# Optimization experiments

Measured on AMD Instinct MI355X. Metric: run time of the kernel, lower is better.

## Reference

```python
import jax, jax.numpy as jnp
import numpy as np

WIN = (7, 7)
HW = WIN[0] * WIN[1]          # 49
C = 128
NUM_HEAD = 4
HEAD_DIM = C // NUM_HEAD
SCALE = HEAD_DIM ** -0.5
BS = 16384
NUM_WIN = 1024


def _relative_position_index():
    coords = np.stack(np.meshgrid(np.arange(WIN[0]), np.arange(WIN[1]), indexing='ij'))
    coords = coords.reshape(2, -1)                      # (2, hw)
    rel = coords[:, :, None] - coords[:, None, :]       # (2, hw, hw)
    rel = rel.transpose(1, 2, 0).copy()                 # (hw, hw, 2)
    rel[:, :, 0] += WIN[0] - 1
    rel[:, :, 1] += WIN[1] - 1
    rel[:, :, 0] *= 2 * WIN[1] - 1
    return rel.sum(-1).astype(np.int32)                 # (hw, hw)


def setup_inputs() -> dict:
    key = jax.random.key(0)
    ks = jax.random.split(key, 7)
    x = jax.random.normal(ks[0], (BS, HW, C), dtype=jnp.float32)
    mask = jax.random.normal(ks[1], (NUM_WIN, HW, HW), dtype=jnp.float32)
    qkv_w = jax.random.normal(ks[2], (3 * C, C), dtype=jnp.float32) * (C ** -0.5)
    qkv_b = jnp.zeros((3 * C,), dtype=jnp.float32)
    proj_w = jax.random.normal(ks[3], (C, C), dtype=jnp.float32) * (C ** -0.5)
    proj_b = jnp.zeros((C,), dtype=jnp.float32)
    num_rel = (2 * WIN[0] - 1) * (2 * WIN[1] - 1)       # 169
    bias_table = jax.random.normal(ks[4], (num_rel, NUM_HEAD), dtype=jnp.float32) * 0.02
    rel_index = jnp.asarray(_relative_position_index())
    return {"x": x, "mask": mask, "qkv_w": qkv_w, "qkv_b": qkv_b,
            "proj_w": proj_w, "proj_b": proj_b, "bias_table": bias_table,
            "rel_index": rel_index}


def reference(x, mask, qkv_w, qkv_b, proj_w, proj_b, bias_table, rel_index):
    bs, hw, c = x.shape
    qkv = x @ qkv_w.T + qkv_b                                   # (bs, hw, 3C)
    qkv = qkv.reshape(bs, hw, 3, NUM_HEAD, HEAD_DIM)
    qkv = jnp.transpose(qkv, (2, 0, 3, 1, 4))                   # (3, bs, H, hw, hd)
    q, k, v = qkv[0] * SCALE, qkv[1], qkv[2]
    attn = jnp.einsum('bhqd,bhkd->bhqk', q, k)                  # (bs, H, hw, hw)
    # gathered relative position bias: (hw, hw, H) -> (H, hw, hw)
    rel_bias = bias_table[rel_index.reshape(-1)].reshape(hw, hw, NUM_HEAD)
    attn = attn + jnp.transpose(rel_bias, (2, 0, 1))[None]
    nW = mask.shape[0]
    attn = attn.reshape(bs // nW, nW, NUM_HEAD, hw, hw) + mask[None, :, None]
    attn = attn.reshape(bs, NUM_HEAD, hw, hw)
    attn = jax.nn.softmax(attn, axis=-1)
    out = jnp.einsum('bhqk,bhkd->bhqd', attn, v)                # (bs, H, hw, hd)
    out = jnp.transpose(out, (0, 2, 1, 3)).reshape(bs, hw, c)
    return out @ proj_w.T + proj_b
```

## Files before the change

kernel.cpp:

```cpp
#include <hip/hip_runtime.h>
#include <hip/hip_bf16.h>

#define THREADS 512
#define WPB 8
#define NWIN 16384
#define NBLK (NWIN / WPB)

typedef short bf16x8 __attribute__((ext_vector_type(8)));
typedef float f32x4 __attribute__((ext_vector_type(4)));

#define XAP 136
#define QKP 264
#define VTP 72

#define XA0_OFF 0
#define XA1_OFF 6664
#define QK_OFF  13328
#define VT_OFF  26264
#define POOL_USHORTS 35480

#define LOG2E 1.4426950408889634f
#define SCALE_Q 0.17677669529663689f

#define COMB_FLOATS (1024 * 4 * 49 * 52)
#define COMB_BYTES  ((size_t)COMB_FLOATS * 4)
#define WQ_USHORTS (96 * 64 * 8)
#define WP_USHORTS (32 * 64 * 8)

static __device__ __forceinline__ unsigned short f2bf(float x) {
    union { __hip_bfloat16 b; unsigned short u; } c;
    c.b = __float2bfloat16(x);
    return c.u;
}
static __device__ __forceinline__ unsigned pack2bf(float lo, float hi) {
    return (unsigned)f2bf(lo) | ((unsigned)f2bf(hi) << 16);
}
static __device__ __forceinline__ ushort4 cvt4(float4 v) {
    ushort4 u; u.x = f2bf(v.x); u.y = f2bf(v.y); u.z = f2bf(v.z); u.w = f2bf(v.w);
    return u;
}

__global__ __launch_bounds__(512)
void prep_weights(const float* __restrict__ qkv_w, const float* __restrict__ proj_w,
                  unsigned short* __restrict__ wq, unsigned short* __restrict__ wp)
{
    const int t = blockIdx.x * 512 + threadIdx.x;
    if (t < 96 * 64) {
        const int lane = t & 63, g = t >> 6;
        const int l16 = lane & 15, lg = lane >> 4;
        const int ks = g & 3, wn = g >> 2;
        const int ch = wn * 16 + l16;
        const float s = (ch < 128) ? (SCALE_Q * LOG2E) : 1.0f;
        const float* p = qkv_w + (size_t)ch * 128 + ks * 32 + lg * 8;
        bf16x8 f;
#pragma unroll
        for (int j = 0; j < 8; ++j) f[j] = (short)f2bf(p[j] * s);
        *(bf16x8*)&wq[(size_t)t * 8] = f;
    } else if (t < 96 * 64 + 32 * 64) {
        const int t2 = t - 96 * 64;
        const int lane = t2 & 63, g = t2 >> 6;
        const int l16 = lane & 15, lg = lane >> 4;
        const int ks = g & 3, wv = g >> 2;
        const float* p = proj_w + (size_t)(wv * 16 + l16) * 128 + ks * 32 + lg * 8;
        bf16x8 f;
#pragma unroll
        for (int j = 0; j < 8; ++j) f[j] = (short)f2bf(p[j]);
        *(bf16x8*)&wp[(size_t)t2 * 8] = f;
    }
}

__global__ __launch_bounds__(512)
void prep_comb(const float* __restrict__ mask, const float* __restrict__ bias_table,
               const int* __restrict__ rel_index, float* __restrict__ comb)
{
    const unsigned t = blockIdx.x * 512 + threadIdx.x;
    if (t >= 1024u * 4u * 49u * 49u) return;
    const unsigned wi = t / 9604u;
    const unsigned r1 = t - wi * 9604u;
    const unsigned h  = r1 / 2401u;
    const unsigned r2 = r1 - h * 2401u;
    const unsigned qt = r2 / 49u;
    const unsigned kt = r2 - qt * 49u;
    const float m = mask[wi * 2401u + r2];
    const float b = bias_table[rel_index[r2] * 4 + h];
    comb[(((size_t)wi * 4u + h) * 49u + qt) * 52u + kt] = (m + b) * LOG2E;
}

__global__ __launch_bounds__(THREADS, 4)
void winattn_kernel(const float* __restrict__ x, const float* __restrict__ comb,
                    const unsigned short* __restrict__ wq, const unsigned short* __restrict__ wpr,
                    const float* __restrict__ qkv_b, const float* __restrict__ proj_b,
                    float* __restrict__ out)
{
    __shared__ __align__(16) unsigned short pool[POOL_USHORTS];

    const int tid  = threadIdx.x;
    const int wave = tid >> 6;
    const int lane = tid & 63;
    const int lg   = lane >> 4;
    const int l16  = lane & 15;
    const int h    = wave >> 1;
    const int mh   = wave & 1;

    const float4 pb = *(const float4*)(proj_b + wave * 16 + lg * 4);

    const int idxA = l16 + 2 * (lane & 16);
    const int idxB = idxA + 16;
    const bool hiSel = (lane & 32) != 0;

    const int win0 = blockIdx.x * WPB;

    {
        unsigned* p32 = (unsigned*)pool;
        for (int i = QK_OFF / 2 + tid; i < (QK_OFF + 12936 + 9216) / 2; i += THREADS)
            p32[i] = 0;
    }
#pragma unroll
    for (int it = 0; it < 4; ++it) {
        const int e = it * 2048 + tid * 4;
        if (e < 6272) {
            float4 v = *(const float4*)(x + (size_t)win0 * 6272 + e);
            *(ushort4*)&pool[XA0_OFF + (e >> 7) * XAP + (e & 127)] = cvt4(v);
        }
    }
    __syncthreads();

    for (int w = 0; w < WPB; ++w) {
        const int win = win0 + w;
        const bool pf = (w + 1 < WPB);
        const int xaC = (w & 1) ? XA1_OFF : XA0_OFF;
        const int xaN = (w & 1) ? XA0_OFF : XA1_OFF;

        if (pf) {
            const float* xp1 = x + (size_t)(win + 1) * 6272;
#pragma unroll
            for (int it = 0; it < 4; ++it) {
                const int e = it * 2048 + tid * 4;
                if (e < 6272) {
                    float4 v = *(const float4*)(xp1 + e);
                    *(ushort4*)&pool[xaN + (e >> 7) * XAP + (e & 127)] = cvt4(v);
                }
            }
        }

        {
            uintptr_t wqu = (uintptr_t)wq;
            asm volatile("" : "+s"(wqu));
            const unsigned short* wqx = (const unsigned short*)wqu;
#pragma unroll
            for (int nt = 0; nt < 3; ++nt) {
                bf16x8 wB[4];
#pragma unroll
                for (int ks = 0; ks < 4; ++ks)
                    wB[ks] = *(const bf16x8*)&wqx[(size_t)(((wave * 3 + nt) * 4 + ks) * 64 + lane) * 8];
                const int chB = wave * 48 + nt * 16;
                float4 qb4;
                if (chB < 256) {
                    qb4 = *(const float4*)(qkv_b + chB + lg * 4);
                    if (chB < 128) { qb4.x *= SCALE_Q * LOG2E; qb4.y *= SCALE_Q * LOG2E;
                                     qb4.z *= SCALE_Q * LOG2E; qb4.w *= SCALE_Q * LOG2E; }
                } else {
                    qb4.x = qkv_b[chB + l16];
                }
#pragma unroll
                for (int mt = 0; mt < 4; ++mt) {
                    bf16x8 xf[4];
#pragma unroll
                    for (int ks = 0; ks < 4; ++ks)
                        xf[ks] = *(const bf16x8*)&pool[xaC + (mt * 16 + l16) * XAP + ks * 32 + lg * 8];
                    f32x4 acc = (f32x4){0.f, 0.f, 0.f, 0.f};
                    if (chB < 256) {
#pragma unroll
                        for (int ks = 0; ks < 4; ++ks)
                            acc = __builtin_amdgcn_mfma_f32_16x16x32_bf16(wB[ks], xf[ks], acc, 0, 0, 0);
                        const int tok = mt * 16 + l16;
                        if (tok < 49) {
                            float4 v; v.x = acc[0] + qb4.x; v.y = acc[1] + qb4.y;
                            v.z = acc[2] + qb4.z; v.w = acc[3] + qb4.w;
                            *(ushort4*)&pool[QK_OFF + tok * QKP + chB + lg * 4] = cvt4(v);
                        }
                    } else {
#pragma unroll
                        for (int ks = 0; ks < 4; ++ks)
                            acc = __builtin_amdgcn_mfma_f32_16x16x32_bf16(xf[ks], wB[ks], acc, 0, 0, 0);
                        const float vb = qb4.x;
                        float4 v; v.x = acc[0] + vb; v.y = acc[1] + vb;
                        v.z = acc[2] + vb; v.w = acc[3] + vb;
                        *(ushort4*)&pool[VT_OFF + (chB - 256 + l16) * VTP + mt * 16 + lg * 4] = cvt4(v);
                    }
                }
            }
        }
        __syncthreads();

        const float* combW = comb + ((size_t)((win & 1023) * 4 + h)) * (49 * 52);
        float inv[2];
        unsigned pk[2][4][2];
#pragma unroll
        for (int nt = 0; nt < 2; ++nt) {
            const int qt = mh * 32 + nt * 16 + l16;
            const int qrow = (qt > 48) ? 48 : qt;
            const float* crow = combW + qrow * 52;
            const float4 c0 = *(const float4*)(crow + lg * 4);
            const float4 c1 = *(const float4*)(crow + 16 + lg * 4);
            const float4 c2 = *(const float4*)(crow + 32 + lg * 4);
            const float  c3 = crow[48];
            const bf16x8 bq = *(const bf16x8*)&pool[QK_OFF + qt * QKP + h * 32 + lg * 8];
            f32x4 S[4];
            __builtin_amdgcn_s_setprio(1);
#pragma unroll
            for (int mt = 0; mt < 4; ++mt) {
                const bf16x8 ak = *(const bf16x8*)&pool[QK_OFF + (mt * 16 + l16) * QKP + 128 + h * 32 + lg * 8];
                S[mt] = __builtin_amdgcn_mfma_f32_16x16x32_bf16(ak, bq, (f32x4){0.f,0.f,0.f,0.f}, 0, 0, 0);
            }
            __builtin_amdgcn_s_setprio(0);
            float lv[12];
            lv[0] = S[0][0] + c0.x; lv[1] = S[0][1] + c0.y;
            lv[2] = S[0][2] + c0.z; lv[3] = S[0][3] + c0.w;
            lv[4] = S[1][0] + c1.x; lv[5] = S[1][1] + c1.y;
            lv[6] = S[1][2] + c1.z; lv[7] = S[1][3] + c1.w;
            lv[8] = S[2][0] + c2.x; lv[9] = S[2][1] + c2.y;
            lv[10] = S[2][2] + c2.z; lv[11] = S[2][3] + c2.w;
            const float lv3 = (lg == 0) ? (S[3][0] + c3) : -1e30f;

            float sum = 0.f;
#pragma unroll
            for (int i = 0; i < 12; ++i) {
                const float p = exp2f(lv[i]);
                lv[i] = p;
                sum += p;
            }
            const float p3 = exp2f(lv3);
            sum += p3;
            sum += __shfl_xor(sum, 16);
            sum += __shfl_xor(sum, 32);
            inv[nt] = 1.0f / sum;
            pk[nt][0][0] = pack2bf(lv[0], lv[1]);  pk[nt][0][1] = pack2bf(lv[2], lv[3]);
            pk[nt][1][0] = pack2bf(lv[4], lv[5]);  pk[nt][1][1] = pack2bf(lv[6], lv[7]);
            pk[nt][2][0] = pack2bf(lv[8], lv[9]);  pk[nt][2][1] = pack2bf(lv[10], lv[11]);
            pk[nt][3][0] = pack2bf(p3, 0.f);       pk[nt][3][1] = 0u;
        }

        f32x4 O[2][2];
#pragma unroll
        for (int i = 0; i < 2; ++i)
#pragma unroll
            for (int j = 0; j < 2; ++j) O[i][j] = (f32x4){0.f, 0.f, 0.f, 0.f};
#pragma unroll
        for (int kh = 0; kh < 2; ++kh) {
            bf16x8 bv[2];
#pragma unroll
            for (int i = 0; i < 2; ++i)
                bv[i] = *(const bf16x8*)&pool[VT_OFF + (h * 32 + i * 16 + l16) * VTP + kh * 32 + lg * 8];
#pragma unroll
            for (int j = 0; j < 2; ++j) {
                const unsigned s0a = (unsigned)__shfl((int)pk[j][2 * kh + 0][0], idxA, 64);
                const unsigned s0b = (unsigned)__shfl((int)pk[j][2 * kh + 1][0], idxA, 64);
                const unsigned s1a = (unsigned)__shfl((int)pk[j][2 * kh + 0][1], idxA, 64);
                const unsigned s1b = (unsigned)__shfl((int)pk[j][2 * kh + 1][1], idxA, 64);
                const unsigned s2a = (unsigned)__shfl((int)pk[j][2 * kh + 0][0], idxB, 64);
                const unsigned s2b = (unsigned)__shfl((int)pk[j][2 * kh + 1][0], idxB, 64);
                const unsigned s3a = (unsigned)__shfl((int)pk[j][2 * kh + 0][1], idxB, 64);
                const unsigned s3b = (unsigned)__shfl((int)pk[j][2 * kh + 1][1], idxB, 64);
                unsigned pau[4];
                pau[0] = hiSel ? s0b : s0a;
                pau[1] = hiSel ? s1b : s1a;
                pau[2] = hiSel ? s2b : s2a;
                pau[3] = hiSel ? s3b : s3a;
                const bf16x8 pa = *(const bf16x8*)pau;
                __builtin_amdgcn_s_setprio(1);
#pragma unroll
                for (int i = 0; i < 2; ++i)
                    O[i][j] = __builtin_amdgcn_mfma_f32_16x16x32_bf16(bv[i], pa, O[i][j], 0, 0, 0);
                __builtin_amdgcn_s_setprio(0);
            }
        }
#pragma unroll
        for (int j = 0; j < 2; ++j) {
            const int tok = mh * 32 + j * 16 + l16;
            if (tok < 49) {
#pragma unroll
                for (int i = 0; i < 2; ++i) {
                    float4 v;
                    v.x = O[i][j][0] * inv[j]; v.y = O[i][j][1] * inv[j];
                    v.z = O[i][j][2] * inv[j]; v.w = O[i][j][3] * inv[j];
                    *(ushort4*)&pool[xaC + tok * XAP + h * 32 + i * 16 + lg * 4] = cvt4(v);
                }
            }
        }
        __syncthreads();

        bf16x8 wp_[4];
        {
            uintptr_t wpu = (uintptr_t)wpr;
            asm volatile("" : "+s"(wpu));
            const unsigned short* wpx = (const unsigned short*)wpu;
#pragma unroll
            for (int ks = 0; ks < 4; ++ks)
                wp_[ks] = *(const bf16x8*)&wpx[(size_t)((wave * 4 + ks) * 64 + lane) * 8];
        }
#pragma unroll
        for (int nt4 = 0; nt4 < 4; ++nt4) {
            f32x4 pc = (f32x4){0.f, 0.f, 0.f, 0.f};
#pragma unroll
            for (int ks = 0; ks < 4; ++ks) {
                const bf16x8 bfr = *(const bf16x8*)&pool[xaC + (nt4 * 16 + l16) * XAP + ks * 32 + lg * 8];
                pc = __builtin_amdgcn_mfma_f32_16x16x32_bf16(wp_[ks], bfr, pc, 0, 0, 0);
            }
            const int tok = nt4 * 16 + l16;
            if (tok < 49) {
                float4 o;
                o.x = pc[0] + pb.x; o.y = pc[1] + pb.y;
                o.z = pc[2] + pb.z; o.w = pc[3] + pb.w;
                *(float4*)(out + ((size_t)win * 49 + tok) * 128 + wave * 16 + lg * 4) = o;
            }
        }
        __syncthreads();
    }
}

extern "C" void kernel_launch(void* const* d_in, const int* in_sizes, int n_in,
                              void* d_out, int out_size, void* d_ws, size_t ws_size,
                              hipStream_t stream) {
    const float* x          = (const float*)d_in[0];
    const float* mask       = (const float*)d_in[1];
    const float* qkv_w      = (const float*)d_in[2];
    const float* qkv_b      = (const float*)d_in[3];
    const float* proj_w     = (const float*)d_in[4];
    const float* proj_b     = (const float*)d_in[5];
    const float* bias_table = (const float*)d_in[6];
    const int*   rel_index  = (const int*)d_in[7];
    float* out = (float*)d_out;
    (void)in_sizes; (void)n_in; (void)ws_size; (void)out_size;

    float* comb = (float*)d_ws;
    unsigned short* wq = (unsigned short*)((char*)d_ws + COMB_BYTES);
    unsigned short* wp = wq + WQ_USHORTS;

    prep_weights<<<dim3(16), dim3(512), 0, stream>>>(qkv_w, proj_w, wq, wp);
    prep_comb<<<dim3(19208), dim3(512), 0, stream>>>(mask, bias_table, rel_index, comb);
    winattn_kernel<<<dim3(NBLK), dim3(THREADS), 0, stream>>>(
        x, comb, wq, wp, qkv_b, proj_b, out);
}
```

Baseline: 421.4 us.

## Single-buffer x tile with XOR-swizzled LDS and register prefetch for higher occupancy

```diff
diff --git a/kernel.cpp b/kernel.cpp
--- a/kernel.cpp
+++ b/kernel.cpp
@@ -9,15 +9,16 @@
 typedef short bf16x8 __attribute__((ext_vector_type(8)));
 typedef float f32x4 __attribute__((ext_vector_type(4)));
 
-#define XAP 136
-#define QKP 264
-#define VTP 72
-
-#define XA0_OFF 0
-#define XA1_OFF 6664
-#define QK_OFF  13328
-#define VT_OFF  26264
-#define POOL_USHORTS 35480
+#define XAP2 128
+#define QKP2 256
+#define VTP2 64
+
+#define XA_OFF 0
+#define QK_OFF 6272
+#define VT_OFF 18816
+#define POOL_USHORTS 27008
+
+#define SWZ(i, r) ((i) ^ (((r) & 7) << 3))
 
 #define LOG2E 1.4426950408889634f
 #define SCALE_Q 0.17677669529663689f
@@ -86,7 +87,7 @@
     comb[(((size_t)wi * 4u + h) * 49u + qt) * 52u + kt] = (m + b) * LOG2E;
 }
 
-__global__ __launch_bounds__(THREADS, 4)
+__global__ __launch_bounds__(THREADS, 6)
 void winattn_kernel(const float* __restrict__ x, const float* __restrict__ comb,
                     const unsigned short* __restrict__ wq, const unsigned short* __restrict__ wpr,
                     const float* __restrict__ qkv_b, const float* __restrict__ proj_b,
@@ -112,7 +113,7 @@
 
     {
         unsigned* p32 = (unsigned*)pool;
-        for (int i = QK_OFF / 2 + tid; i < (QK_OFF + 12936 + 9216) / 2; i += THREADS)
+        for (int i = QK_OFF / 2 + tid; i < POOL_USHORTS / 2; i += THREADS)
             p32[i] = 0;
     }
 #pragma unroll
@@ -120,7 +121,7 @@
         const int e = it * 2048 + tid * 4;
         if (e < 6272) {
             float4 v = *(const float4*)(x + (size_t)win0 * 6272 + e);
-            *(ushort4*)&pool[XA0_OFF + (e >> 7) * XAP + (e & 127)] = cvt4(v);
+            *(ushort4*)&pool[SWZ(e, e >> 7)] = cvt4(v);
         }
     }
     __syncthreads();
@@ -128,18 +129,14 @@
     for (int w = 0; w < WPB; ++w) {
         const int win = win0 + w;
         const bool pf = (w + 1 < WPB);
-        const int xaC = (w & 1) ? XA1_OFF : XA0_OFF;
-        const int xaN = (w & 1) ? XA0_OFF : XA1_OFF;
-
+
+        float4 xr[4];
         if (pf) {
             const float* xp1 = x + (size_t)(win + 1) * 6272;
 #pragma unroll
             for (int it = 0; it < 4; ++it) {
                 const int e = it * 2048 + tid * 4;
-                if (e < 6272) {
-                    float4 v = *(const float4*)(xp1 + e);
-                    *(ushort4*)&pool[xaN + (e >> 7) * XAP + (e & 127)] = cvt4(v);
-                }
+                if (e < 6272) xr[it] = *(const float4*)(xp1 + e);
             }
         }
 
@@ -164,10 +161,11 @@
                 }
 #pragma unroll
                 for (int mt = 0; mt < 4; ++mt) {
+                    const int xrow = mt * 16 + l16;
                     bf16x8 xf[4];
 #pragma unroll
                     for (int ks = 0; ks < 4; ++ks)
-                        xf[ks] = *(const bf16x8*)&pool[xaC + (mt * 16 + l16) * XAP + ks * 32 + lg * 8];
+                        xf[ks] = *(const bf16x8*)&pool[SWZ(XA_OFF + xrow * XAP2 + ks * 32 + lg * 8, xrow)];
                     f32x4 acc = (f32x4){0.f, 0.f, 0.f, 0.f};
                     if (chB < 256) {
 #pragma unroll
@@ -177,21 +175,28 @@
                         if (tok < 49) {
                             float4 v; v.x = acc[0] + qb4.x; v.y = acc[1] + qb4.y;
                             v.z = acc[2] + qb4.z; v.w = acc[3] + qb4.w;
-                            *(ushort4*)&pool[QK_OFF + tok * QKP + chB + lg * 4] = cvt4(v);
+                            *(ushort4*)&pool[SWZ(QK_OFF + tok * QKP2 + chB + lg * 4, tok)] = cvt4(v);
                         }
                     } else {
 #pragma unroll
                         for (int ks = 0; ks < 4; ++ks)
                             acc = __builtin_amdgcn_mfma_f32_16x16x32_bf16(xf[ks], wB[ks], acc, 0, 0, 0);
                         const float vb = qb4.x;
+                        const int vrow = chB - 256 + l16;
                         float4 v; v.x = acc[0] + vb; v.y = acc[1] + vb;
                         v.z = acc[2] + vb; v.w = acc[3] + vb;
-                        *(ushort4*)&pool[VT_OFF + (chB - 256 + l16) * VTP + mt * 16 + lg * 4] = cvt4(v);
+                        *(ushort4*)&pool[SWZ(VT_OFF + vrow * VTP2 + mt * 16 + lg * 4, vrow)] = cvt4(v);
                     }
                 }
             }
         }
         __syncthreads();
+
+        ushort4 xb[4];
+        if (pf) {
+#pragma unroll
+            for (int it = 0; it < 4; ++it) xb[it] = cvt4(xr[it]);
+        }
 
         const float* combW = comb + ((size_t)((win & 1023) * 4 + h)) * (49 * 52);
         float inv[2];
@@ -205,12 +210,13 @@
             const float4 c1 = *(const float4*)(crow + 16 + lg * 4);
             const float4 c2 = *(const float4*)(crow + 32 + lg * 4);
             const float  c3 = crow[48];
-            const bf16x8 bq = *(const bf16x8*)&pool[QK_OFF + qt * QKP + h * 32 + lg * 8];
+            const bf16x8 bq = *(const bf16x8*)&pool[SWZ(QK_OFF + qt * QKP2 + h * 32 + lg * 8, qt)];
             f32x4 S[4];
             __builtin_amdgcn_s_setprio(1);
 #pragma unroll
             for (int mt = 0; mt < 4; ++mt) {
-                const bf16x8 ak = *(const bf16x8*)&pool[QK_OFF + (mt * 16 + l16) * QKP + 128 + h * 32 + lg * 8];
+                const int ar = mt * 16 + l16;
+                const bf16x8 ak = *(const bf16x8*)&pool[SWZ(QK_OFF + ar * QKP2 + 128 + h * 32 + lg * 8, ar)];
                 S[mt] = __builtin_amdgcn_mfma_f32_16x16x32_bf16(ak, bq, (f32x4){0.f,0.f,0.f,0.f}, 0, 0, 0);
             }
             __builtin_amdgcn_s_setprio(0);
@@ -250,8 +256,10 @@
         for (int kh = 0; kh < 2; ++kh) {
             bf16x8 bv[2];
 #pragma unroll
-            for (int i = 0; i < 2; ++i)
-                bv[i] = *(const bf16x8*)&pool[VT_OFF + (h * 32 + i * 16 + l16) * VTP + kh * 32 + lg * 8];
+            for (int i = 0; i < 2; ++i) {
+                const int br = h * 32 + i * 16 + l16;
+                bv[i] = *(const bf16x8*)&pool[SWZ(VT_OFF + br * VTP2 + kh * 32 + lg * 8, br)];
+            }
 #pragma unroll
             for (int j = 0; j < 2; ++j) {
                 const unsigned s0a = (unsigned)__shfl((int)pk[j][2 * kh + 0][0], idxA, 64);
@@ -284,7 +292,7 @@
                     float4 v;
                     v.x = O[i][j][0] * inv[j]; v.y = O[i][j][1] * inv[j];
                     v.z = O[i][j][2] * inv[j]; v.w = O[i][j][3] * inv[j];
-                    *(ushort4*)&pool[xaC + tok * XAP + h * 32 + i * 16 + lg * 4] = cvt4(v);
+                    *(ushort4*)&pool[SWZ(XA_OFF + tok * XAP2 + h * 32 + i * 16 + lg * 4, tok)] = cvt4(v);
                 }
             }
         }
@@ -301,18 +309,28 @@
         }
 #pragma unroll
         for (int nt4 = 0; nt4 < 4; ++nt4) {
+            const int tr = nt4 * 16 + l16;
             f32x4 pc = (f32x4){0.f, 0.f, 0.f, 0.f};
 #pragma unroll
             for (int ks = 0; ks < 4; ++ks) {
-                const bf16x8 bfr = *(const bf16x8*)&pool[xaC + (nt4 * 16 + l16) * XAP + ks * 32 + lg * 8];
+                const bf16x8 bfr = *(const bf16x8*)&pool[SWZ(XA_OFF + tr * XAP2 + ks * 32 + lg * 8, tr)];
                 pc = __builtin_amdgcn_mfma_f32_16x16x32_bf16(wp_[ks], bfr, pc, 0, 0, 0);
             }
-            const int tok = nt4 * 16 + l16;
-            if (tok < 49) {
+            if (tr < 49) {
                 float4 o;
                 o.x = pc[0] + pb.x; o.y = pc[1] + pb.y;
                 o.z = pc[2] + pb.z; o.w = pc[3] + pb.w;
-                *(float4*)(out + ((size_t)win * 49 + tok) * 128 + wave * 16 + lg * 4) = o;
+                *(float4*)(out + ((size_t)win * 49 + tr) * 128 + wave * 16 + lg * 4) = o;
+            }
+        }
+        __syncthreads();
+
+        if (pf) {
+#pragma unroll
+            for (int it = 0; it < 4; ++it) {
+                const int e = it * 2048 + tid * 4;
+                if (e < 6272)
+                    *(ushort4*)&pool[SWZ(e, e >> 7)] = xb[it];
             }
         }
         __syncthreads();
```

Result: slower. 954.3 us (+126.5%).

## Assign one wave per head, keep Q in registers, shrink LDS footprint

Applied to the files above, without the earlier changes.

```diff
diff --git a/kernel.cpp b/kernel.cpp
--- a/kernel.cpp
+++ b/kernel.cpp
@@ -1,7 +1,7 @@
 #include <hip/hip_runtime.h>
 #include <hip/hip_bf16.h>
 
-#define THREADS 512
+#define THREADS 256
 #define WPB 8
 #define NWIN 16384
 #define NBLK (NWIN / WPB)
@@ -9,15 +9,13 @@
 typedef short bf16x8 __attribute__((ext_vector_type(8)));
 typedef float f32x4 __attribute__((ext_vector_type(4)));
 
-#define XAP 136
-#define QKP 264
-#define VTP 72
-
-#define XA0_OFF 0
-#define XA1_OFF 6664
-#define QK_OFF  13328
-#define VT_OFF  26264
-#define POOL_USHORTS 35480
+#define XP 136
+#define KP 136
+#define VTP 52
+#define X_OFF 0
+#define K_OFF 6664
+#define VT_OFF 13328
+#define POOL_USHORTS 20016
 
 #define LOG2E 1.4426950408889634f
 #define SCALE_Q 0.17677669529663689f
@@ -95,14 +93,10 @@
     __shared__ __align__(16) unsigned short pool[POOL_USHORTS];
 
     const int tid  = threadIdx.x;
-    const int wave = tid >> 6;
+    const int h    = tid >> 6;
     const int lane = tid & 63;
     const int lg   = lane >> 4;
     const int l16  = lane & 15;
-    const int h    = wave >> 1;
-    const int mh   = wave & 1;
-
-    const float4 pb = *(const float4*)(proj_b + wave * 16 + lg * 4);
 
     const int idxA = l16 + 2 * (lane & 16);
     const int idxB = idxA + 16;
@@ -112,15 +106,14 @@
 
     {
         unsigned* p32 = (unsigned*)pool;
-        for (int i = QK_OFF / 2 + tid; i < (QK_OFF + 12936 + 9216) / 2; i += THREADS)
-            p32[i] = 0;
+        for (int i = K_OFF / 2 + tid; i < POOL_USHORTS / 2; i += THREADS) p32[i] = 0;
     }
 #pragma unroll
-    for (int it = 0; it < 4; ++it) {
-        const int e = it * 2048 + tid * 4;
+    for (int it = 0; it < 7; ++it) {
+        const int e = it * 1024 + tid * 4;
         if (e < 6272) {
             float4 v = *(const float4*)(x + (size_t)win0 * 6272 + e);
-            *(ushort4*)&pool[XA0_OFF + (e >> 7) * XAP + (e & 127)] = cvt4(v);
+            *(ushort4*)&pool[X_OFF + (e >> 7) * XP + (e & 127)] = cvt4(v);
         }
     }
     __syncthreads();
@@ -128,191 +121,218 @@
     for (int w = 0; w < WPB; ++w) {
         const int win = win0 + w;
         const bool pf = (w + 1 < WPB);
-        const int xaC = (w & 1) ? XA1_OFF : XA0_OFF;
-        const int xaN = (w & 1) ? XA0_OFF : XA1_OFF;
+
+        uintptr_t wqu = (uintptr_t)wq;
+        asm volatile("" : "+s"(wqu));
+        const unsigned short* wqx = (const unsigned short*)wqu;
+
+#pragma unroll
+        for (int nt = 0; nt < 2; ++nt) {
+            bf16x8 wB[4];
+#pragma unroll
+            for (int ks = 0; ks < 4; ++ks)
+                wB[ks] = *(const bf16x8*)&wqx[(size_t)(((8 + 2 * h + nt) * 4 + ks) * 64 + lane) * 8];
+            const float4 kb = *(const float4*)(qkv_b + 128 + h * 32 + nt * 16 + lg * 4);
+#pragma unroll
+            for (int mt = 0; mt < 4; ++mt) {
+                bf16x8 xf[4];
+#pragma unroll
+                for (int ks = 0; ks < 4; ++ks)
+                    xf[ks] = *(const bf16x8*)&pool[X_OFF + (mt * 16 + l16) * XP + ks * 32 + lg * 8];
+                f32x4 acc = (f32x4){0.f, 0.f, 0.f, 0.f};
+#pragma unroll
+                for (int ks = 0; ks < 4; ++ks)
+                    acc = __builtin_amdgcn_mfma_f32_16x16x32_bf16(wB[ks], xf[ks], acc, 0, 0, 0);
+                const int tok = mt * 16 + l16;
+                if (tok < 49) {
+                    float4 v; v.x = acc[0] + kb.x; v.y = acc[1] + kb.y;
+                    v.z = acc[2] + kb.z; v.w = acc[3] + kb.w;
+                    *(ushort4*)&pool[K_OFF + tok * KP + h * 32 + nt * 16 + lg * 4] = cvt4(v);
+                }
+            }
+        }
+#pragma unroll
+        for (int nt = 0; nt < 2; ++nt) {
+            bf16x8 wB[4];
+#pragma unroll
+            for (int ks = 0; ks < 4; ++ks)
+                wB[ks] = *(const bf16x8*)&wqx[(size_t)(((16 + 2 * h + nt) * 4 + ks) * 64 + lane) * 8];
+            const float vb = qkv_b[256 + h * 32 + nt * 16 + l16];
+#pragma unroll
+            for (int mt = 0; mt < 4; ++mt) {
+                bf16x8 xf[4];
+#pragma unroll
+                for (int ks = 0; ks < 4; ++ks)
+                    xf[ks] = *(const bf16x8*)&pool[X_OFF + (mt * 16 + l16) * XP + ks * 32 + lg * 8];
+                f32x4 acc = (f32x4){0.f, 0.f, 0.f, 0.f};
+#pragma unroll
+                for (int ks = 0; ks < 4; ++ks)
+                    acc = __builtin_amdgcn_mfma_f32_16x16x32_bf16(xf[ks], wB[ks], acc, 0, 0, 0);
+                const int vcol = mt * 16 + lg * 4;
+                if (vcol <= 48) {
+                    float4 v; v.x = acc[0] + vb; v.y = acc[1] + vb;
+                    v.z = acc[2] + vb; v.w = acc[3] + vb;
+                    *(ushort4*)&pool[VT_OFF + (h * 32 + nt * 16 + l16) * VTP + vcol] = cvt4(v);
+                }
+            }
+        }
+        unsigned qP[4][2][2];
+#pragma unroll
+        for (int nt = 0; nt < 2; ++nt) {
+            bf16x8 wB[4];
+#pragma unroll
+            for (int ks = 0; ks < 4; ++ks)
+                wB[ks] = *(const bf16x8*)&wqx[(size_t)(((2 * h + nt) * 4 + ks) * 64 + lane) * 8];
+            float4 qb = *(const float4*)(qkv_b + h * 32 + nt * 16 + lg * 4);
+            qb.x *= SCALE_Q * LOG2E; qb.y *= SCALE_Q * LOG2E;
+            qb.z *= SCALE_Q * LOG2E; qb.w *= SCALE_Q * LOG2E;
+#pragma unroll
+            for (int tq = 0; tq < 4; ++tq) {
+                bf16x8 xf[4];
+#pragma unroll
+                for (int ks = 0; ks < 4; ++ks)
+                    xf[ks] = *(const bf16x8*)&pool[X_OFF + (tq * 16 + l16) * XP + ks * 32 + lg * 8];
+                f32x4 acc = (f32x4){0.f, 0.f, 0.f, 0.f};
+#pragma unroll
+                for (int ks = 0; ks < 4; ++ks)
+                    acc = __builtin_amdgcn_mfma_f32_16x16x32_bf16(wB[ks], xf[ks], acc, 0, 0, 0);
+                qP[tq][nt][0] = pack2bf(acc[0] + qb.x, acc[1] + qb.y);
+                qP[tq][nt][1] = pack2bf(acc[2] + qb.z, acc[3] + qb.w);
+            }
+        }
+
+        bf16x8 ak[4];
+#pragma unroll
+        for (int mt = 0; mt < 4; ++mt)
+            ak[mt] = *(const bf16x8*)&pool[K_OFF + (mt * 16 + l16) * KP + h * 32 + lg * 8];
+
+        const float* combW = comb + ((size_t)((win & 1023) * 4 + h)) * (49 * 52);
+
+#pragma unroll
+        for (int tq = 0; tq < 4; ++tq) {
+            unsigned bqw[4];
+            {
+                const unsigned a0 = (unsigned)__shfl((int)qP[tq][0][0], idxA, 64);
+                const unsigned a1 = (unsigned)__shfl((int)qP[tq][0][1], idxA, 64);
+                const unsigned a2 = (unsigned)__shfl((int)qP[tq][0][0], idxB, 64);
+                const unsigned a3 = (unsigned)__shfl((int)qP[tq][0][1], idxB, 64);
+                const unsigned b0 = (unsigned)__shfl((int)qP[tq][1][0], idxA, 64);
+                const unsigned b1 = (unsigned)__shfl((int)qP[tq][1][1], idxA, 64);
+                const unsigned b2 = (unsigned)__shfl((int)qP[tq][1][0], idxB, 64);
+                const unsigned b3 = (unsigned)__shfl((int)qP[tq][1][1], idxB, 64);
+                bqw[0] = hiSel ? b0 : a0;
+                bqw[1] = hiSel ? b1 : a1;
+                bqw[2] = hiSel ? b2 : a2;
+                bqw[3] = hiSel ? b3 : a3;
+            }
+            const bf16x8 bq = *(const bf16x8*)bqw;
+            const int qt = tq * 16 + l16;
+            const float* crow = combW + ((qt > 48) ? 48 : qt) * 52;
+
+            f32x4 S[4];
+            __builtin_amdgcn_s_setprio(1);
+#pragma unroll
+            for (int mt = 0; mt < 4; ++mt)
+                S[mt] = __builtin_amdgcn_mfma_f32_16x16x32_bf16(ak[mt], bq, (f32x4){0.f,0.f,0.f,0.f}, 0, 0, 0);
+            __builtin_amdgcn_s_setprio(0);
+
+            float sum = 0.f;
+            unsigned pk[4][2];
+#pragma unroll
+            for (int mt = 0; mt < 3; ++mt) {
+                const float4 c = *(const float4*)(crow + mt * 16 + lg * 4);
+                const float e0 = exp2f(S[mt][0] + c.x);
+                const float e1 = exp2f(S[mt][1] + c.y);
+                const float e2 = exp2f(S[mt][2] + c.z);
+                const float e3 = exp2f(S[mt][3] + c.w);
+                sum += (e0 + e1) + (e2 + e3);
+                pk[mt][0] = pack2bf(e0, e1);
+                pk[mt][1] = pack2bf(e2, e3);
+            }
+            const float e48 = (lg == 0) ? exp2f(S[3][0] + crow[48]) : 0.f;
+            sum += e48;
+            pk[3][0] = pack2bf(e48, 0.f);
+            pk[3][1] = 0u;
+
+            sum += __shfl_xor(sum, 16);
+            sum += __shfl_xor(sum, 32);
+            const float inv = 1.0f / sum;
+
+            f32x4 O0 = (f32x4){0.f,0.f,0.f,0.f}, O1 = (f32x4){0.f,0.f,0.f,0.f};
+#pragma unroll
+            for (int kh = 0; kh < 2; ++kh) {
+                const bf16x8 bv0 = *(const bf16x8*)&pool[VT_OFF + (h * 32 + l16) * VTP + kh * 32 + lg * 8];
+                const bf16x8 bv1 = *(const bf16x8*)&pool[VT_OFF + (h * 32 + 16 + l16) * VTP + kh * 32 + lg * 8];
+                unsigned pau[4];
+                {
+                    const unsigned pa0 = (unsigned)__shfl((int)pk[2 * kh + 0][0], idxA, 64);
+                    const unsigned pa1 = (unsigned)__shfl((int)pk[2 * kh + 0][1], idxA, 64);
+                    const unsigned pa2 = (unsigned)__shfl((int)pk[2 * kh + 0][0], idxB, 64);
+                    const unsigned pa3 = (unsigned)__shfl((int)pk[2 * kh + 0][1], idxB, 64);
+                    const unsigned pb0 = (unsigned)__shfl((int)pk[2 * kh + 1][0], idxA, 64);
+                    const unsigned pb1 = (unsigned)__shfl((int)pk[2 * kh + 1][1], idxA, 64);
+                    const unsigned pb2 = (unsigned)__shfl((int)pk[2 * kh + 1][0], idxB, 64);
+                    const unsigned pb3 = (unsigned)__shfl((int)pk[2 * kh + 1][1], idxB, 64);
+                    pau[0] = hiSel ? pb0 : pa0;
+                    pau[1] = hiSel ? pb1 : pa1;
+                    pau[2] = hiSel ? pb2 : pa2;
+                    pau[3] = hiSel ? pb3 : pa3;
+                }
+                const bf16x8 pa = *(const bf16x8*)pau;
+                __builtin_amdgcn_s_setprio(1);
+                O0 = __builtin_amdgcn_mfma_f32_16x16x32_bf16(bv0, pa, O0, 0, 0, 0);
+                O1 = __builtin_amdgcn_mfma_f32_16x16x32_bf16(bv1, pa, O1, 0, 0, 0);
+                __builtin_amdgcn_s_setprio(0);
+            }
+            const int tok = tq * 16 + l16;
+            if (tok < 49) {
+                float4 v0; v0.x = O0[0] * inv; v0.y = O0[1] * inv; v0.z = O0[2] * inv; v0.w = O0[3] * inv;
+                float4 v1; v1.x = O1[0] * inv; v1.y = O1[1] * inv; v1.z = O1[2] * inv; v1.w = O1[3] * inv;
+                *(ushort4*)&pool[K_OFF + tok * KP + h * 32 + lg * 4]      = cvt4(v0);
+                *(ushort4*)&pool[K_OFF + tok * KP + h * 32 + 16 + lg * 4] = cvt4(v1);
+            }
+        }
+        __syncthreads();
 
         if (pf) {
             const float* xp1 = x + (size_t)(win + 1) * 6272;
 #pragma unroll
-            for (int it = 0; it < 4; ++it) {
-                const int e = it * 2048 + tid * 4;
+            for (int it = 0; it < 7; ++it) {
+                const int e = it * 1024 + tid * 4;
                 if (e < 6272) {
                     float4 v = *(const float4*)(xp1 + e);
-                    *(ushort4*)&pool[xaN + (e >> 7) * XAP + (e & 127)] = cvt4(v);
-                }
-            }
-        }
-
-        {
-            uintptr_t wqu = (uintptr_t)wq;
-            asm volatile("" : "+s"(wqu));
-            const unsigned short* wqx = (const unsigned short*)wqu;
-#pragma unroll
-            for (int nt = 0; nt < 3; ++nt) {
-                bf16x8 wB[4];
-#pragma unroll
-                for (int ks = 0; ks < 4; ++ks)
-                    wB[ks] = *(const bf16x8*)&wqx[(size_t)(((wave * 3 + nt) * 4 + ks) * 64 + lane) * 8];
-                const int chB = wave * 48 + nt * 16;
-                float4 qb4;
-                if (chB < 256) {
-                    qb4 = *(const float4*)(qkv_b + chB + lg * 4);
-                    if (chB < 128) { qb4.x *= SCALE_Q * LOG2E; qb4.y *= SCALE_Q * LOG2E;
-                                     qb4.z *= SCALE_Q * LOG2E; qb4.w *= SCALE_Q * LOG2E; }
-                } else {
-                    qb4.x = qkv_b[chB + l16];
-                }
-#pragma unroll
-                for (int mt = 0; mt < 4; ++mt) {
-                    bf16x8 xf[4];
-#pragma unroll
-                    for (int ks = 0; ks < 4; ++ks)
-                        xf[ks] = *(const bf16x8*)&pool[xaC + (mt * 16 + l16) * XAP + ks * 32 + lg * 8];
-                    f32x4 acc = (f32x4){0.f, 0.f, 0.f, 0.f};
-                    if (chB < 256) {
-#pragma unroll
-                        for (int ks = 0; ks < 4; ++ks)
-                            acc = __builtin_amdgcn_mfma_f32_16x16x32_bf16(wB[ks], xf[ks], acc, 0, 0, 0);
-                        const int tok = mt * 16 + l16;
-                        if (tok < 49) {
-                            float4 v; v.x = acc[0] + qb4.x; v.y = acc[1] + qb4.y;
-                            v.z = acc[2] + qb4.z; v.w = acc[3] + qb4.w;
-                            *(ushort4*)&pool[QK_OFF + tok * QKP + chB + lg * 4] = cvt4(v);
-                        }
-                    } else {
-#pragma unroll
-                        for (int ks = 0; ks < 4; ++ks)
-                            acc = __builtin_amdgcn_mfma_f32_16x16x32_bf16(xf[ks], wB[ks], acc, 0, 0, 0);
-                        const float vb = qb4.x;
-                        float4 v; v.x = acc[0] + vb; v.y = acc[1] + vb;
-                        v.z = acc[2] + vb; v.w = acc[3] + vb;
-                        *(ushort4*)&pool[VT_OFF + (chB - 256 + l16) * VTP + mt * 16 + lg * 4] = cvt4(v);
-                    }
-                }
-            }
-        }
-        __syncthreads();
-
-        const float* combW = comb + ((size_t)((win & 1023) * 4 + h)) * (49 * 52);
-        float inv[2];
-        unsigned pk[2][4][2];
-#pragma unroll
-        for (int nt = 0; nt < 2; ++nt) {
-            const int qt = mh * 32 + nt * 16 + l16;
-            const int qrow = (qt > 48) ? 48 : qt;
-            const float* crow = combW + qrow * 52;
-            const float4 c0 = *(const float4*)(crow + lg * 4);
-            const float4 c1 = *(const float4*)(crow + 16 + lg * 4);
-            const float4 c2 = *(const float4*)(crow + 32 + lg * 4);
-            const float  c3 = crow[48];
-            const bf16x8 bq = *(const bf16x8*)&pool[QK_OFF + qt * QKP + h * 32 + lg * 8];
-            f32x4 S[4];
-            __builtin_amdgcn_s_setprio(1);
-#pragma unroll
-            for (int mt = 0; mt < 4; ++mt) {
-                const bf16x8 ak = *(const bf16x8*)&pool[QK_OFF + (mt * 16 + l16) * QKP + 128 + h * 32 + lg * 8];
-                S[mt] = __builtin_amdgcn_mfma_f32_16x16x32_bf16(ak, bq, (f32x4){0.f,0.f,0.f,0.f}, 0, 0, 0);
-            }
-            __builtin_amdgcn_s_setprio(0);
-            float lv[12];
-            lv[0] = S[0][0] + c0.x; lv[1] = S[0][1] + c0.y;
-            lv[2] = S[0][2] + c0.z; lv[3] = S[0][3] + c0.w;
-            lv[4] = S[1][0] + c1.x; lv[5] = S[1][1] + c1.y;
-            lv[6] = S[1][2] + c1.z; lv[7] = S[1][3] + c1.w;
-            lv[8] = S[2][0] + c2.x; lv[9] = S[2][1] + c2.y;
-            lv[10] = S[2][2] + c2.z; lv[11] = S[2][3] + c2.w;
-            const float lv3 = (lg == 0) ? (S[3][0] + c3) : -1e30f;
-
-            float sum = 0.f;
-#pragma unroll
-            for (int i = 0; i < 12; ++i) {
-                const float p = exp2f(lv[i]);
-                lv[i] = p;
-                sum += p;
-            }
-            const float p3 = exp2f(lv3);
-            sum += p3;
-            sum += __shfl_xor(sum, 16);
-            sum += __shfl_xor(sum, 32);
-            inv[nt] = 1.0f / sum;
-            pk[nt][0][0] = pack2bf(lv[0], lv[1]);  pk[nt][0][1] = pack2bf(lv[2], lv[3]);
-            pk[nt][1][0] = pack2bf(lv[4], lv[5]);  pk[nt][1][1] = pack2bf(lv[6], lv[7]);
-            pk[nt][2][0] = pack2bf(lv[8], lv[9]);  pk[nt][2][1] = pack2bf(lv[10], lv[11]);
-            pk[nt][3][0] = pack2bf(p3, 0.f);       pk[nt][3][1] = 0u;
-        }
-
-        f32x4 O[2][2];
-#pragma unroll
-        for (int i = 0; i < 2; ++i)
-#pragma unroll
-            for (int j = 0; j < 2; ++j) O[i][j] = (f32x4){0.f, 0.f, 0.f, 0.f};
-#pragma unroll
-        for (int kh = 0; kh < 2; ++kh) {
-            bf16x8 bv[2];
-#pragma unroll
-            for (int i = 0; i < 2; ++i)
-                bv[i] = *(const bf16x8*)&pool[VT_OFF + (h * 32 + i * 16 + l16) * VTP + kh * 32 + lg * 8];
-#pragma unroll
-            for (int j = 0; j < 2; ++j) {
-                const unsigned s0a = (unsigned)__shfl((int)pk[j][2 * kh + 0][0], idxA, 64);
-                const unsigned s0b = (unsigned)__shfl((int)pk[j][2 * kh + 1][0], idxA, 64);
-                const unsigned s1a = (unsigned)__shfl((int)pk[j][2 * kh + 0][1], idxA, 64);
-                const unsigned s1b = (unsigned)__shfl((int)pk[j][2 * kh + 1][1], idxA, 64);
-                const unsigned s2a = (unsigned)__shfl((int)pk[j][2 * kh + 0][0], idxB, 64);
-                const unsigned s2b = (unsigned)__shfl((int)pk[j][2 * kh + 1][0], idxB, 64);
-                const unsigned s3a = (unsigned)__shfl((int)pk[j][2 * kh + 0][1], idxB, 64);
-                const unsigned s3b = (unsigned)__shfl((int)pk[j][2 * kh + 1][1], idxB, 64);
-                unsigned pau[4];
-                pau[0] = hiSel ? s0b : s0a;
-                pau[1] = hiSel ? s1b : s1a;
-                pau[2] = hiSel ? s2b : s2a;
-                pau[3] = hiSel ? s3b : s3a;
-                const bf16x8 pa = *(const bf16x8*)pau;
-                __builtin_amdgcn_s_setprio(1);
-#pragma unroll
-                for (int i = 0; i < 2; ++i)
-                    O[i][j] = __builtin_amdgcn_mfma_f32_16x16x32_bf16(bv[i], pa, O[i][j], 0, 0, 0);
-                __builtin_amdgcn_s_setprio(0);
-            }
-        }
-#pragma unroll
-        for (int j = 0; j < 2; ++j) {
-            const int tok = mh * 32 + j * 16 + l16;
-            if (tok < 49) {
-#pragma unroll
-                for (int i = 0; i < 2; ++i) {
-                    float4 v;
-                    v.x = O[i][j][0] * inv[j]; v.y = O[i][j][1] * inv[j];
-                    v.z = O[i][j][2] * inv[j]; v.w = O[i][j][3] * inv[j];
-                    *(ushort4*)&pool[xaC + tok * XAP + h * 32 + i * 16 + lg * 4] = cvt4(v);
-                }
-            }
-        }
-        __syncthreads();
-
-        bf16x8 wp_[4];
+                    *(ushort4*)&pool[X_OFF + (e >> 7) * XP + (e & 127)] = cvt4(v);
+                }
+            }
+        }
+
         {
             uintptr_t wpu = (uintptr_t)wpr;
             asm volatile("" : "+s"(wpu));
             const unsigned short* wpx = (const unsigned short*)wpu;
 #pragma unroll
-            for (int ks = 0; ks < 4; ++ks)
-                wp_[ks] = *(const bf16x8*)&wpx[(size_t)((wave * 4 + ks) * 64 + lane) * 8];
-        }
-#pragma unroll
-        for (int nt4 = 0; nt4 < 4; ++nt4) {
-            f32x4 pc = (f32x4){0.f, 0.f, 0.f, 0.f};
-#pragma unroll
-            for (int ks = 0; ks < 4; ++ks) {
-                const bf16x8 bfr = *(const bf16x8*)&pool[xaC + (nt4 * 16 + l16) * XAP + ks * 32 + lg * 8];
-                pc = __builtin_amdgcn_mfma_f32_16x16x32_bf16(wp_[ks], bfr, pc, 0, 0, 0);
-            }
-            const int tok = nt4 * 16 + l16;
-            if (tok < 49) {
-                float4 o;
-                o.x = pc[0] + pb.x; o.y = pc[1] + pb.y;
-                o.z = pc[2] + pb.z; o.w = pc[3] + pb.w;
-                *(float4*)(out + ((size_t)win * 49 + tok) * 128 + wave * 16 + lg * 4) = o;
+            for (int wt = 0; wt < 2; ++wt) {
+                bf16x8 wp_[4];
+#pragma unroll
+                for (int ks = 0; ks < 4; ++ks)
+                    wp_[ks] = *(const bf16x8*)&wpx[(size_t)(((2 * h + wt) * 4 + ks) * 64 + lane) * 8];
+                const float4 pbv = *(const float4*)(proj_b + h * 32 + wt * 16 + lg * 4);
+#pragma unroll
+                for (int nt4 = 0; nt4 < 4; ++nt4) {
+                    f32x4 pc = (f32x4){0.f, 0.f, 0.f, 0.f};
+#pragma unroll
+                    for (int ks = 0; ks < 4; ++ks) {
+                        const bf16x8 bfr = *(const bf16x8*)&pool[K_OFF + (nt4 * 16 + l16) * KP + ks * 32 + lg * 8];
+                        pc = __builtin_amdgcn_mfma_f32_16x16x32_bf16(wp_[ks], bfr, pc, 0, 0, 0);
+                    }
+                    const int tok = nt4 * 16 + l16;
+                    if (tok < 49) {
+                        float4 o;
+                        o.x = pc[0] + pbv.x; o.y = pc[1] + pbv.y;
+                        o.z = pc[2] + pbv.z; o.w = pc[3] + pbv.w;
+                        *(float4*)(out + ((size_t)win * 49 + tok) * 128 + h * 32 + wt * 16 + lg * 4) = o;
+                    }
+                }
             }
         }
         __syncthreads();
```

New measurement: 498.2 us. 18.2% more time.
